# Kernel tuning notes

Measured on AMD Instinct MI355X. Metric: run time of the kernel, lower is better.

The kernel has to match this reference:

```python
import jax, jax.numpy as jnp
import numpy as np

WIN = 16  # win_size == stride


def setup_inputs() -> dict:
    key = jax.random.key(0)
    k0, k1, k2 = jax.random.split(key, 3)
    B, M, D, H = 32, 2048, 512, 64  # H = input_size // time_ratio
    return {
        "x": jax.random.normal(k0, (B, M, D), dtype=jnp.float32),
        "W1": jax.random.normal(k1, (D, H), dtype=jnp.float32) / np.sqrt(D).astype(np.float32),
        "b1": jnp.zeros((H,), jnp.float32),
        "W2": jax.random.normal(k2, (H, D), dtype=jnp.float32) / np.sqrt(H).astype(np.float32),
        "b2": jnp.zeros((D,), jnp.float32),
    }


def _softsign(v):
    return v / (1.0 + jnp.abs(v))


def reference(x, W1, b1, W2, b2):
    B, M, D = x.shape
    pad_total = (-M) % WIN
    lo = pad_total // 2
    hi = pad_total - lo
    xp = jnp.pad(x, ((0, 0), (lo, hi), (0, 0)), mode="edge")
    Mp = M + pad_total
    nW = Mp // WIN
    xw = xp.reshape(B, nW, WIN, D)
    m = xw.mean(axis=2)                     # windowed mean-pool -> [B, nW, D]
    h = _softsign(jnp.einsum("bwd,dh->bwh", m, W1) + b1)
    g = jax.nn.sigmoid(_softsign(jnp.einsum("bwh,hd->bwd", h, W2) + b2))  # [B, nW, D]
    y = (xw * g[:, :, None, :]).reshape(B, Mp, D)  # broadcast gate over window
    return y[:, lo:lo + M, :]
```

## Files before the change

### kernel.cpp

```cpp
#include <hip/hip_runtime.h>
#include <cmath>


constexpr int WIN = 16;
constexpr int D   = 512;
constexpr int H   = 64;
constexpr int TPB = 256;

__global__ __launch_bounds__(TPB) void se_block_kernel(
    const float* __restrict__ x,
    const float* __restrict__ W1,
    const float* __restrict__ b1,
    const float* __restrict__ W2,
    const float* __restrict__ b2,
    float* __restrict__ y)
{
    const int tid = threadIdx.x;
    const size_t base = (size_t)blockIdx.x * (size_t)(WIN * D);
    const float4* __restrict__ xw = reinterpret_cast<const float4*>(x + base);
    float4*       __restrict__ yw = reinterpret_cast<float4*>(y + base);

    const float4* __restrict__ W1f4 = reinterpret_cast<const float4*>(W1);
    const float4* __restrict__ W2f4 = reinterpret_cast<const float4*>(W2);

    __shared__ float4 s_ps[TPB];
    __shared__ float  s_hp[16][H];
    __shared__ float  s_h[H];
    __shared__ float  s_gp[2][D];
    __shared__ float  s_g[D];

    float4 r[8];
#pragma unroll
    for (int i = 0; i < 8; ++i) r[i] = xw[i * TPB + tid];

    float4 ps = r[0];
#pragma unroll
    for (int i = 1; i < 8; ++i) {
        ps.x += r[i].x; ps.y += r[i].y; ps.z += r[i].z; ps.w += r[i].w;
    }
    s_ps[tid] = ps;
    __syncthreads();

    {
        const int p  = tid >> 4;
        const int j4 = tid & 15;
        float4 acc = make_float4(0.f, 0.f, 0.f, 0.f);
#pragma unroll 2
        for (int kk4 = 0; kk4 < 8; ++kk4) {
            const int c4 = p * 8 + kk4;
            const float4 a = s_ps[c4];
            const float4 b = s_ps[c4 + 128];
            const float mv0 = a.x + b.x, mv1 = a.y + b.y, mv2 = a.z + b.z, mv3 = a.w + b.w;
            const int k = c4 * 4;
            const float4 w0 = W1f4[(size_t)(k + 0) * 16 + j4];
            const float4 w1 = W1f4[(size_t)(k + 1) * 16 + j4];
            const float4 w2 = W1f4[(size_t)(k + 2) * 16 + j4];
            const float4 w3 = W1f4[(size_t)(k + 3) * 16 + j4];
            acc.x = fmaf(mv0, w0.x, acc.x); acc.y = fmaf(mv0, w0.y, acc.y);
            acc.z = fmaf(mv0, w0.z, acc.z); acc.w = fmaf(mv0, w0.w, acc.w);
            acc.x = fmaf(mv1, w1.x, acc.x); acc.y = fmaf(mv1, w1.y, acc.y);
            acc.z = fmaf(mv1, w1.z, acc.z); acc.w = fmaf(mv1, w1.w, acc.w);
            acc.x = fmaf(mv2, w2.x, acc.x); acc.y = fmaf(mv2, w2.y, acc.y);
            acc.z = fmaf(mv2, w2.z, acc.z); acc.w = fmaf(mv2, w2.w, acc.w);
            acc.x = fmaf(mv3, w3.x, acc.x); acc.y = fmaf(mv3, w3.y, acc.y);
            acc.z = fmaf(mv3, w3.z, acc.z); acc.w = fmaf(mv3, w3.w, acc.w);
        }
        const float sc = 1.0f / 16.0f;
        s_hp[p][j4 * 4 + 0] = acc.x * sc;
        s_hp[p][j4 * 4 + 1] = acc.y * sc;
        s_hp[p][j4 * 4 + 2] = acc.z * sc;
        s_hp[p][j4 * 4 + 3] = acc.w * sc;
    }
    __syncthreads();

    if (tid < H) {
        float s = b1[tid];
#pragma unroll
        for (int p = 0; p < 16; ++p) s += s_hp[p][tid];
        s_h[tid] = s / (1.0f + fabsf(s));
    }
    __syncthreads();

    {
        const int q  = tid >> 7;
        const int d4 = tid & 127;
        const float4* __restrict__ s_h4 = reinterpret_cast<const float4*>(s_h);
        float4 acc = make_float4(0.f, 0.f, 0.f, 0.f);
#pragma unroll 2
        for (int jj4 = 0; jj4 < 8; ++jj4) {
            const float4 hv = s_h4[q * 8 + jj4];
            const int j = (q * 8 + jj4) * 4;
            const float4 w0 = W2f4[(size_t)(j + 0) * 128 + d4];
            const float4 w1 = W2f4[(size_t)(j + 1) * 128 + d4];
            const float4 w2 = W2f4[(size_t)(j + 2) * 128 + d4];
            const float4 w3 = W2f4[(size_t)(j + 3) * 128 + d4];
            acc.x = fmaf(hv.x, w0.x, acc.x); acc.y = fmaf(hv.x, w0.y, acc.y);
            acc.z = fmaf(hv.x, w0.z, acc.z); acc.w = fmaf(hv.x, w0.w, acc.w);
            acc.x = fmaf(hv.y, w1.x, acc.x); acc.y = fmaf(hv.y, w1.y, acc.y);
            acc.z = fmaf(hv.y, w1.z, acc.z); acc.w = fmaf(hv.y, w1.w, acc.w);
            acc.x = fmaf(hv.z, w2.x, acc.x); acc.y = fmaf(hv.z, w2.y, acc.y);
            acc.z = fmaf(hv.z, w2.z, acc.z); acc.w = fmaf(hv.z, w2.w, acc.w);
            acc.x = fmaf(hv.w, w3.x, acc.x); acc.y = fmaf(hv.w, w3.y, acc.y);
            acc.z = fmaf(hv.w, w3.z, acc.z); acc.w = fmaf(hv.w, w3.w, acc.w);
        }
        s_gp[q][d4 * 4 + 0] = acc.x;
        s_gp[q][d4 * 4 + 1] = acc.y;
        s_gp[q][d4 * 4 + 2] = acc.z;
        s_gp[q][d4 * 4 + 3] = acc.w;
    }
    __syncthreads();

    {
        const float2 bb = reinterpret_cast<const float2*>(b2)[tid];
        const int d = tid * 2;
        float sx = s_gp[0][d]     + s_gp[1][d]     + bb.x;
        float sy = s_gp[0][d + 1] + s_gp[1][d + 1] + bb.y;
        sx = sx / (1.0f + fabsf(sx));
        sy = sy / (1.0f + fabsf(sy));
        reinterpret_cast<float2*>(s_g)[tid] =
            make_float2(1.0f / (1.0f + __expf(-sx)), 1.0f / (1.0f + __expf(-sy)));
    }
    __syncthreads();

    const float4 g = reinterpret_cast<const float4*>(s_g)[tid & 127];
#pragma unroll
    for (int i = 0; i < 8; ++i) {
        float4 o;
        o.x = r[i].x * g.x;
        o.y = r[i].y * g.y;
        o.z = r[i].z * g.z;
        o.w = r[i].w * g.w;
        yw[i * TPB + tid] = o;
    }
}

extern "C" void kernel_launch(void* const* d_in, const int* in_sizes, int n_in,
                              void* d_out, int out_size, void* d_ws, size_t ws_size,
                              hipStream_t stream) {
    const float* x  = (const float*)d_in[0];
    const float* W1 = (const float*)d_in[1];
    const float* b1 = (const float*)d_in[2];
    const float* W2 = (const float*)d_in[3];
    const float* b2 = (const float*)d_in[4];
    float* y = (float*)d_out;

    const int n_windows = in_sizes[0] / (WIN * D);
    se_block_kernel<<<dim3(n_windows), dim3(TPB), 0, stream>>>(x, W1, b1, W2, b2, y);
}
```

Baseline: 59.84 us.

## Process four windows per block to amortize weight loads; re-read x and use nontemporal stores

Each block now handles four windows, so the W1/W2 weight reads are shared across four mean vectors in both small GEMVs, and the grid shrinks by a factor of four. The input tile is no longer held in registers. It is read twice, once for pooling and again from global or L2 for the gated multiply, and the output uses nontemporal stores. The tradeoffs are extra global reads of x, fewer blocks to hide latency, and more shared memory per block.

New measurement: 73.06 us. +22.1%, slower.

```diff
diff --git a/kernel.cpp b/kernel.cpp
--- a/kernel.cpp
+++ b/kernel.cpp
@@ -6,6 +6,9 @@
 constexpr int D   = 512;
 constexpr int H   = 64;
 constexpr int TPB = 256;
+constexpr int NW  = 4;
+
+typedef float v4f __attribute__((ext_vector_type(4)));
 
 __global__ __launch_bounds__(TPB) void se_block_kernel(
     const float* __restrict__ x,
@@ -16,121 +19,165 @@
     float* __restrict__ y)
 {
     const int tid = threadIdx.x;
-    const size_t base = (size_t)blockIdx.x * (size_t)(WIN * D);
+    const size_t base = (size_t)blockIdx.x * (size_t)(NW * WIN * D);
     const float4* __restrict__ xw = reinterpret_cast<const float4*>(x + base);
-    float4*       __restrict__ yw = reinterpret_cast<float4*>(y + base);
+    v4f*          __restrict__ yw = reinterpret_cast<v4f*>(y + base);
 
     const float4* __restrict__ W1f4 = reinterpret_cast<const float4*>(W1);
     const float4* __restrict__ W2f4 = reinterpret_cast<const float4*>(W2);
+    const float4* __restrict__ b2f4 = reinterpret_cast<const float4*>(b2);
 
-    __shared__ float4 s_ps[TPB];
-    __shared__ float  s_hp[16][H];
-    __shared__ float  s_h[H];
-    __shared__ float  s_gp[2][D];
-    __shared__ float  s_g[D];
+    __shared__ __align__(16) char s_bufA[16 * 1024];
+    __shared__ __align__(16) float s_m[NW][D];
+    __shared__ __align__(16) float s_h[NW][H];
+    __shared__ __align__(16) float s_g[NW][D];
 
-    float4 r[8];
+    float4* s_m4 = reinterpret_cast<float4*>(&s_m[0][0]);
+    float4* s_h4 = reinterpret_cast<float4*>(&s_h[0][0]);
+    float4* s_g4 = reinterpret_cast<float4*>(&s_g[0][0]);
+
+    {
+        float4* s_ps = reinterpret_cast<float4*>(s_bufA);
 #pragma unroll
-    for (int i = 0; i < 8; ++i) r[i] = xw[i * TPB + tid];
-
-    float4 ps = r[0];
+        for (int w = 0; w < NW; ++w) {
+            float4 ps = make_float4(0.f, 0.f, 0.f, 0.f);
 #pragma unroll
-    for (int i = 1; i < 8; ++i) {
-        ps.x += r[i].x; ps.y += r[i].y; ps.z += r[i].z; ps.w += r[i].w;
+            for (int i = 0; i < 8; ++i) {
+                const float4 v = xw[w * 2048 + i * TPB + tid];
+                ps.x += v.x; ps.y += v.y; ps.z += v.z; ps.w += v.w;
+            }
+            s_ps[w * TPB + tid] = ps;
+        }
+        __syncthreads();
+#pragma unroll
+        for (int rep = 0; rep < 2; ++rep) {
+            const int idx = rep * TPB + tid;
+            const int w  = idx >> 7;
+            const int c  = idx & 127;
+            const float4 a = s_ps[w * TPB + c];
+            const float4 b = s_ps[w * TPB + c + 128];
+            float4 m;
+            const float sc = 1.0f / 16.0f;
+            m.x = (a.x + b.x) * sc; m.y = (a.y + b.y) * sc;
+            m.z = (a.z + b.z) * sc; m.w = (a.w + b.w) * sc;
+            s_m4[w * 128 + c] = m;
+        }
     }
-    s_ps[tid] = ps;
     __syncthreads();
 
     {
+        float4* s_hp4 = reinterpret_cast<float4*>(s_bufA);
         const int p  = tid >> 4;
         const int j4 = tid & 15;
-        float4 acc = make_float4(0.f, 0.f, 0.f, 0.f);
+        float4 acc[NW];
+#pragma unroll
+        for (int w = 0; w < NW; ++w) acc[w] = make_float4(0.f, 0.f, 0.f, 0.f);
 #pragma unroll 2
         for (int kk4 = 0; kk4 < 8; ++kk4) {
             const int c4 = p * 8 + kk4;
-            const float4 a = s_ps[c4];
-            const float4 b = s_ps[c4 + 128];
-            const float mv0 = a.x + b.x, mv1 = a.y + b.y, mv2 = a.z + b.z, mv3 = a.w + b.w;
-            const int k = c4 * 4;
+            const int k  = c4 * 4;
             const float4 w0 = W1f4[(size_t)(k + 0) * 16 + j4];
             const float4 w1 = W1f4[(size_t)(k + 1) * 16 + j4];
             const float4 w2 = W1f4[(size_t)(k + 2) * 16 + j4];
             const float4 w3 = W1f4[(size_t)(k + 3) * 16 + j4];
-            acc.x = fmaf(mv0, w0.x, acc.x); acc.y = fmaf(mv0, w0.y, acc.y);
-            acc.z = fmaf(mv0, w0.z, acc.z); acc.w = fmaf(mv0, w0.w, acc.w);
-            acc.x = fmaf(mv1, w1.x, acc.x); acc.y = fmaf(mv1, w1.y, acc.y);
-            acc.z = fmaf(mv1, w1.z, acc.z); acc.w = fmaf(mv1, w1.w, acc.w);
-            acc.x = fmaf(mv2, w2.x, acc.x); acc.y = fmaf(mv2, w2.y, acc.y);
-            acc.z = fmaf(mv2, w2.z, acc.z); acc.w = fmaf(mv2, w2.w, acc.w);
-            acc.x = fmaf(mv3, w3.x, acc.x); acc.y = fmaf(mv3, w3.y, acc.y);
-            acc.z = fmaf(mv3, w3.z, acc.z); acc.w = fmaf(mv3, w3.w, acc.w);
+#pragma unroll
+            for (int w = 0; w < NW; ++w) {
+                const float4 mv = s_m4[w * 128 + c4];
+                acc[w].x = fmaf(mv.x, w0.x, acc[w].x); acc[w].y = fmaf(mv.x, w0.y, acc[w].y);
+                acc[w].z = fmaf(mv.x, w0.z, acc[w].z); acc[w].w = fmaf(mv.x, w0.w, acc[w].w);
+                acc[w].x = fmaf(mv.y, w1.x, acc[w].x); acc[w].y = fmaf(mv.y, w1.y, acc[w].y);
+                acc[w].z = fmaf(mv.y, w1.z, acc[w].z); acc[w].w = fmaf(mv.y, w1.w, acc[w].w);
+                acc[w].x = fmaf(mv.z, w2.x, acc[w].x); acc[w].y = fmaf(mv.z, w2.y, acc[w].y);
+                acc[w].z = fmaf(mv.z, w2.z, acc[w].z); acc[w].w = fmaf(mv.z, w2.w, acc[w].w);
+                acc[w].x = fmaf(mv.w, w3.x, acc[w].x); acc[w].y = fmaf(mv.w, w3.y, acc[w].y);
+                acc[w].z = fmaf(mv.w, w3.z, acc[w].z); acc[w].w = fmaf(mv.w, w3.w, acc[w].w);
+            }
         }
-        const float sc = 1.0f / 16.0f;
-        s_hp[p][j4 * 4 + 0] = acc.x * sc;
-        s_hp[p][j4 * 4 + 1] = acc.y * sc;
-        s_hp[p][j4 * 4 + 2] = acc.z * sc;
-        s_hp[p][j4 * 4 + 3] = acc.w * sc;
-    }
-    __syncthreads();
-
-    if (tid < H) {
-        float s = b1[tid];
 #pragma unroll
-        for (int p = 0; p < 16; ++p) s += s_hp[p][tid];
-        s_h[tid] = s / (1.0f + fabsf(s));
+        for (int w = 0; w < NW; ++w) s_hp4[(p * NW + w) * 16 + j4] = acc[w];
     }
     __syncthreads();
 
     {
+        const float* s_hp = reinterpret_cast<const float*>(s_bufA);
+        const int w = tid >> 6;
+        const int j = tid & 63;
+        float s = b1[j];
+#pragma unroll
+        for (int p = 0; p < 16; ++p) s += s_hp[(p * NW + w) * 64 + j];
+        s_h[w][j] = s / (1.0f + fabsf(s));
+    }
+    __syncthreads();
+
+    {
+        float4* s_gp4 = reinterpret_cast<float4*>(s_bufA);
         const int q  = tid >> 7;
         const int d4 = tid & 127;
-        const float4* __restrict__ s_h4 = reinterpret_cast<const float4*>(s_h);
-        float4 acc = make_float4(0.f, 0.f, 0.f, 0.f);
+        float4 acc[NW];
+#pragma unroll
+        for (int w = 0; w < NW; ++w) acc[w] = make_float4(0.f, 0.f, 0.f, 0.f);
 #pragma unroll 2
         for (int jj4 = 0; jj4 < 8; ++jj4) {
-            const float4 hv = s_h4[q * 8 + jj4];
-            const int j = (q * 8 + jj4) * 4;
+            const int jg = q * 8 + jj4;
+            const int j  = jg * 4;
             const float4 w0 = W2f4[(size_t)(j + 0) * 128 + d4];
             const float4 w1 = W2f4[(size_t)(j + 1) * 128 + d4];
             const float4 w2 = W2f4[(size_t)(j + 2) * 128 + d4];
             const float4 w3 = W2f4[(size_t)(j + 3) * 128 + d4];
-            acc.x = fmaf(hv.x, w0.x, acc.x); acc.y = fmaf(hv.x, w0.y, acc.y);
-            acc.z = fmaf(hv.x, w0.z, acc.z); acc.w = fmaf(hv.x, w0.w, acc.w);
-            acc.x = fmaf(hv.y, w1.x, acc.x); acc.y = fmaf(hv.y, w1.y, acc.y);
-            acc.z = fmaf(hv.y, w1.z, acc.z); acc.w = fmaf(hv.y, w1.w, acc.w);
-            acc.x = fmaf(hv.z, w2.x, acc.x); acc.y = fmaf(hv.z, w2.y, acc.y);
-            acc.z = fmaf(hv.z, w2.z, acc.z); acc.w = fmaf(hv.z, w2.w, acc.w);
-            acc.x = fmaf(hv.w, w3.x, acc.x); acc.y = fmaf(hv.w, w3.y, acc.y);
-            acc.z = fmaf(hv.w, w3.z, acc.z); acc.w = fmaf(hv.w, w3.w, acc.w);
+#pragma unroll
+            for (int w = 0; w < NW; ++w) {
+                const float4 hv = s_h4[w * 16 + jg];
+                acc[w].x = fmaf(hv.x, w0.x, acc[w].x); acc[w].y = fmaf(hv.x, w0.y, acc[w].y);
+                acc[w].z = fmaf(hv.x, w0.z, acc[w].z); acc[w].w = fmaf(hv.x, w0.w, acc[w].w);
+                acc[w].x = fmaf(hv.y, w1.x, acc[w].x); acc[w].y = fmaf(hv.y, w1.y, acc[w].y);
+                acc[w].z = fmaf(hv.y, w1.z, acc[w].z); acc[w].w = fmaf(hv.y, w1.w, acc[w].w);
+                acc[w].x = fmaf(hv.z, w2.x, acc[w].x); acc[w].y = fmaf(hv.z, w2.y, acc[w].y);
+                acc[w].z = fmaf(hv.z, w2.z, acc[w].z); acc[w].w = fmaf(hv.z, w2.w, acc[w].w);
+                acc[w].x = fmaf(hv.w, w3.x, acc[w].x); acc[w].y = fmaf(hv.w, w3.y, acc[w].y);
+                acc[w].z = fmaf(hv.w, w3.z, acc[w].z); acc[w].w = fmaf(hv.w, w3.w, acc[w].w);
+            }
         }
-        s_gp[q][d4 * 4 + 0] = acc.x;
-        s_gp[q][d4 * 4 + 1] = acc.y;
-        s_gp[q][d4 * 4 + 2] = acc.z;
-        s_gp[q][d4 * 4 + 3] = acc.w;
+#pragma unroll
+        for (int w = 0; w < NW; ++w) s_gp4[(q * NW + w) * 128 + d4] = acc[w];
     }
     __syncthreads();
 
     {
-        const float2 bb = reinterpret_cast<const float2*>(b2)[tid];
-        const int d = tid * 2;
-        float sx = s_gp[0][d]     + s_gp[1][d]     + bb.x;
-        float sy = s_gp[0][d + 1] + s_gp[1][d + 1] + bb.y;
-        sx = sx / (1.0f + fabsf(sx));
-        sy = sy / (1.0f + fabsf(sy));
-        reinterpret_cast<float2*>(s_g)[tid] =
-            make_float2(1.0f / (1.0f + __expf(-sx)), 1.0f / (1.0f + __expf(-sy)));
+        const float4* s_gp4 = reinterpret_cast<const float4*>(s_bufA);
+#pragma unroll
+        for (int rep = 0; rep < 2; ++rep) {
+            const int idx = rep * TPB + tid;
+            const int w  = idx >> 7;
+            const int d4 = idx & 127;
+            const float4 a = s_gp4[(0 * NW + w) * 128 + d4];
+            const float4 b = s_gp4[(1 * NW + w) * 128 + d4];
+            const float4 bb = b2f4[d4];
+            float4 s;
+            s.x = a.x + b.x + bb.x; s.y = a.y + b.y + bb.y;
+            s.z = a.z + b.z + bb.z; s.w = a.w + b.w + bb.w;
+            s.x = s.x / (1.0f + fabsf(s.x)); s.y = s.y / (1.0f + fabsf(s.y));
+            s.z = s.z / (1.0f + fabsf(s.z)); s.w = s.w / (1.0f + fabsf(s.w));
+            float4 g;
+            g.x = 1.0f / (1.0f + __expf(-s.x)); g.y = 1.0f / (1.0f + __expf(-s.y));
+            g.z = 1.0f / (1.0f + __expf(-s.z)); g.w = 1.0f / (1.0f + __expf(-s.w));
+            s_g4[w * 128 + d4] = g;
+        }
     }
     __syncthreads();
 
-    const float4 g = reinterpret_cast<const float4*>(s_g)[tid & 127];
+    {
+        const int c = tid & 127;
 #pragma unroll
-    for (int i = 0; i < 8; ++i) {
-        float4 o;
-        o.x = r[i].x * g.x;
-        o.y = r[i].y * g.y;
-        o.z = r[i].z * g.z;
-        o.w = r[i].w * g.w;
-        yw[i * TPB + tid] = o;
+        for (int w = 0; w < NW; ++w) {
+            const float4 g = s_g4[w * 128 + c];
+#pragma unroll
+            for (int i = 0; i < 8; ++i) {
+                const float4 v = xw[w * 2048 + i * TPB + tid];
+                v4f o;
+                o.x = v.x * g.x; o.y = v.y * g.y; o.z = v.z * g.z; o.w = v.w * g.w;
+                __builtin_nontemporal_store(o, &yw[w * 2048 + i * TPB + tid]);
+            }
+        }
     }
 }
 
@@ -145,5 +192,6 @@
     float* y = (float*)d_out;
 
     const int n_windows = in_sizes[0] / (WIN * D);
-    se_block_kernel<<<dim3(n_windows), dim3(TPB), 0, stream>>>(x, W1, b1, W2, b2, y);
+    const int n_blocks  = n_windows / NW;
+    se_block_kernel<<<dim3(n_blocks), dim3(TPB), 0, stream>>>(x, W1, b1, W2, b2, y);
 }
```
